# Kernel optimization log

Measured on AMD Instinct MI355X. Metric: run time of the kernel, lower is better.

## Reference

```python
import jax, jax.numpy as jnp
import numpy as np

DIM = 512
NUM_HEADS = 8
HEAD_DIM = DIM // NUM_HEADS
SCALE = HEAD_DIM ** -0.5


def setup_inputs() -> dict:
    key = jax.random.key(0)
    k_x, k_qkv, k_proj, k_pb = jax.random.split(key, 4)
    x = jax.random.normal(k_x, (2, 4096, DIM), dtype=jnp.float32)
    # nn.Linear weights: stored as [out, in]; qkv_bias=False so no qkv bias.
    w_qkv = jax.random.normal(k_qkv, (3 * DIM, DIM), dtype=jnp.float32) * (DIM ** -0.5)
    w_proj = jax.random.normal(k_proj, (DIM, DIM), dtype=jnp.float32) * (DIM ** -0.5)
    b_proj = jax.random.normal(k_pb, (DIM,), dtype=jnp.float32) * 0.01
    return {"x": x, "w_qkv": w_qkv, "w_proj": w_proj, "b_proj": b_proj}


def reference(x, w_qkv, w_proj, b_proj):
    B, N, D = x.shape
    H, Hd = NUM_HEADS, HEAD_DIM
    # qkv: [B, N, 3D] -> [3, B, H, N, Hd]
    qkv = (x @ w_qkv.T).reshape(B, N, 3, H, Hd).transpose(2, 0, 3, 1, 4)
    q, k, v = qkv[0], qkv[1], qkv[2]
    # Naive full attention matrix in fp32 (matches original non-fused path).
    attn = jnp.einsum('bhqd,bhkd->bhqk', q, k) * SCALE
    attn = jax.nn.softmax(attn, axis=-1)
    out = jnp.einsum('bhqk,bhkd->bhqd', attn, v)
    out = out.transpose(0, 2, 1, 3).reshape(B, N, D)
    return out @ w_proj.T + b_proj
```

## Files before the change

### kernel.cpp

```cpp
#include <hip/hip_runtime.h>
#include <stdint.h>

#define SEQ   4096
#define DIMM  512
#define HDIM  64
#define NH    8
#define ROWS  8192
#define QKVN  1536

typedef __attribute__((ext_vector_type(8))) __bf16 bf16x8;
typedef __attribute__((ext_vector_type(4))) float  f32x4;
typedef __attribute__((ext_vector_type(2))) uint32_t u32x2;

__device__ __forceinline__ uint16_t f2bfu(float f) {
  uint32_t u = __builtin_bit_cast(uint32_t, f);
  return (uint16_t)((u + 0x7FFFu + ((u >> 16) & 1u)) >> 16);
}

__device__ __forceinline__ f32x4 mfma16(bf16x8 a, bf16x8 b, f32x4 c) {
  return __builtin_amdgcn_mfma_f32_16x16x32_bf16(a, b, c, 0, 0, 0);
}

#if __has_builtin(__builtin_amdgcn_exp2f)
#define EXP2F(x) __builtin_amdgcn_exp2f(x)
#else
#define EXP2F(x) exp2f(x)
#endif

__device__ __forceinline__ void gld16(const void* g, void* l) {
  __builtin_amdgcn_global_load_lds(
      (const __attribute__((address_space(1))) uint32_t*)g,
      (__attribute__((address_space(3))) uint32_t*)l, 16, 0, 0);
}

#define X4  (ROWS * DIMM / 4)
#define Q4  (QKVN * DIMM / 4)
#define P4  (DIMM * DIMM / 4)

__global__ __launch_bounds__(256) void cvt_kernel(
    const float* __restrict__ x, const float* __restrict__ wq,
    const float* __restrict__ wp, uint16_t* __restrict__ xb,
    uint16_t* __restrict__ wqb, uint16_t* __restrict__ wpb) {
  int idx = blockIdx.x * 256 + threadIdx.x;
  const float* src; uint16_t* dst; int i4;
  if (idx < X4)            { src = x;  dst = xb;  i4 = idx; }
  else if (idx < X4 + Q4)  { src = wq; dst = wqb; i4 = idx - X4; }
  else                     { src = wp; dst = wpb; i4 = idx - X4 - Q4; }
  float4 v = ((const float4*)src)[i4];
  ushort4 o;
  o.x = f2bfu(v.x); o.y = f2bfu(v.y); o.z = f2bfu(v.z); o.w = f2bfu(v.w);
  ((ushort4*)dst)[i4] = o;
}

__device__ __forceinline__ void gemm_core(
    const uint16_t* __restrict__ A, const uint16_t* __restrict__ B,
    uint16_t* As, uint16_t* Bs, f32x4 acc[4][4]) {
  const int tid = threadIdx.x;
  const int lane = tid & 63, wave = tid >> 6;
  const int quad = lane >> 4, l16 = lane & 15;
  const int wr = (wave & 1) * 64, wc = (wave >> 1) * 64;
  const int bm = blockIdx.x, bn = blockIdx.y;
  const int sw = (l16 >> 1) & 3;

  for (int kt = 0; kt < DIMM / 32; ++kt) {
#pragma unroll
    for (int it = 0; it < 2; ++it) {
      int L = it * 256 + tid;
      int r = L >> 2, c = L & 3;
      int gc = c ^ ((r >> 1) & 3);
      int ldsoff = (it * 256 + (tid & ~63)) * 16;
      gld16((const char*)A + ((size_t)(bm * 128 + r) * DIMM + kt * 32) * 2 + gc * 16,
            (char*)As + ldsoff);
      gld16((const char*)B + ((size_t)(bn * 128 + r) * DIMM + kt * 32) * 2 + gc * 16,
            (char*)Bs + ldsoff);
    }
    __syncthreads();
    bf16x8 af[4], bfr[4];
#pragma unroll
    for (int i = 0; i < 4; ++i)
      af[i] = *(const bf16x8*)(As + (wr + i * 16 + l16) * 32 + ((quad ^ sw) * 8));
#pragma unroll
    for (int j = 0; j < 4; ++j)
      bfr[j] = *(const bf16x8*)(Bs + (wc + j * 16 + l16) * 32 + ((quad ^ sw) * 8));
#pragma unroll
    for (int i = 0; i < 4; ++i)
#pragma unroll
      for (int j = 0; j < 4; ++j)
        acc[i][j] = mfma16(af[i], bfr[j], acc[i][j]);
    __syncthreads();
  }
}

__global__ __launch_bounds__(256, 2) void qkv_gemm(
    const uint16_t* __restrict__ xb, const uint16_t* __restrict__ wqb,
    uint16_t* __restrict__ qd, uint16_t* __restrict__ kd,
    uint16_t* __restrict__ vt) {
  __shared__ __align__(16) uint16_t As[128 * 32];
  __shared__ __align__(16) uint16_t Bs[128 * 32];
  f32x4 acc[4][4];
#pragma unroll
  for (int i = 0; i < 4; ++i)
#pragma unroll
    for (int j = 0; j < 4; ++j) acc[i][j] = f32x4{0.f, 0.f, 0.f, 0.f};

  gemm_core(xb, wqb, As, Bs, acc);

  const int lane = threadIdx.x & 63, wave = threadIdx.x >> 6;
  const int quad = lane >> 4, l16 = lane & 15;
  const int wr = (wave & 1) * 64, wc = (wave >> 1) * 64;
  const float qscale = 0.125f * 1.44269504f;
#pragma unroll
  for (int i = 0; i < 4; ++i) {
    int m0 = blockIdx.x * 128 + wr + i * 16 + quad * 4;
    int b = m0 >> 12, n0 = m0 & 4095;
#pragma unroll
    for (int j = 0; j < 4; ++j) {
      int jc = blockIdx.y * 128 + wc + j * 16 + l16;
      int region = jc >> 9;
      int h = (jc >> 6) & 7, hd = jc & 63;
      int bh = (b << 3) | h;
      if (region == 0) {
#pragma unroll
        for (int r = 0; r < 4; ++r)
          qd[((size_t)bh * SEQ + n0 + r) * HDIM + hd] = f2bfu(acc[i][j][r] * qscale);
      } else if (region == 1) {
#pragma unroll
        for (int r = 0; r < 4; ++r)
          kd[((size_t)bh * SEQ + n0 + r) * HDIM + hd] = f2bfu(acc[i][j][r]);
      } else {
        ushort4 pk;
        pk.x = f2bfu(acc[i][j][0]); pk.y = f2bfu(acc[i][j][1]);
        pk.z = f2bfu(acc[i][j][2]); pk.w = f2bfu(acc[i][j][3]);
        *(ushort4*)(vt + ((size_t)bh * HDIM + hd) * SEQ + n0) = pk;
      }
    }
  }
}

__global__ __launch_bounds__(512, 4) void attn_kernel(
    const uint16_t* __restrict__ qd, const uint16_t* __restrict__ kd,
    const uint16_t* __restrict__ vt, uint16_t* __restrict__ ao) {
  __shared__ __align__(16) uint16_t Ks[128 * 64];
  __shared__ __align__(16) uint16_t Vs[64 * 128];
  __shared__ __align__(16) uint16_t Ps[8][32 * 64];

  const int tid = threadIdx.x, lane = tid & 63, wave = tid >> 6;
  const int quad = lane >> 4, l16 = lane & 15;
  const int pair = wave >> 1, khalf = wave & 1;
  const int qt = blockIdx.x, bh = blockIdx.y;
  const size_t base_qk = (size_t)bh * SEQ * HDIM;
  const size_t base_v  = (size_t)bh * HDIM * SEQ;
  const int sw7 = l16 & 7;
  char* Pw = (char*)Ps + wave * 4096;

  bf16x8 qf[2][2];
#pragma unroll
  for (int it2 = 0; it2 < 2; ++it2)
#pragma unroll
    for (int kh = 0; kh < 2; ++kh)
      qf[it2][kh] = *(const bf16x8*)(qd + base_qk +
          (size_t)(qt * 128 + pair * 32 + it2 * 16 + l16) * HDIM + kh * 32 + quad * 8);

  f32x4 O[2][4];
  float lsum[2] = {0.f, 0.f};
#pragma unroll
  for (int a = 0; a < 2; ++a)
#pragma unroll
    for (int d = 0; d < 4; ++d) O[a][d] = f32x4{0.f, 0.f, 0.f, 0.f};

  for (int kt = 0; kt < SEQ / 128; ++kt) {
#pragma unroll
    for (int it = 0; it < 2; ++it) {
      int L = it * 512 + tid;
      int ldsoff = (it * 512 + (tid & ~63)) * 16;
      int rk = L >> 3, ck = L & 7;
      int gck = ck ^ (rk & 7);
      gld16((const char*)kd + (base_qk + (size_t)(kt * 128 + rk) * HDIM) * 2 + gck * 16,
            (char*)Ks + ldsoff);
      int rv = L >> 4, cv = L & 15;
      int gcv = cv ^ (rv & 15);
      gld16((const char*)vt + (base_v + (size_t)rv * SEQ + (size_t)kt * 128) * 2 + gcv * 16,
            (char*)Vs + ldsoff);
    }
    __syncthreads();

    f32x4 P[4][2];
#pragma unroll
    for (int jh = 0; jh < 4; ++jh) {
      int jf = khalf * 4 + jh;
      const uint16_t* krow = Ks + (jf * 16 + l16) * 64;
      bf16x8 kf0 = *(const bf16x8*)(krow + ((quad ^ sw7) * 8));
      bf16x8 kf1 = *(const bf16x8*)(krow + (((4 + quad) ^ sw7) * 8));
#pragma unroll
      for (int it2 = 0; it2 < 2; ++it2) {
        f32x4 s = f32x4{0.f, 0.f, 0.f, 0.f};
        s = mfma16(kf0, qf[it2][0], s);
        s = mfma16(kf1, qf[it2][1], s);
        P[jh][it2] = s;
      }
    }

#pragma unroll
    for (int jh = 0; jh < 4; ++jh)
#pragma unroll
      for (int it2 = 0; it2 < 2; ++it2) {
        float p0 = EXP2F(P[jh][it2][0]);
        float p1 = EXP2F(P[jh][it2][1]);
        float p2 = EXP2F(P[jh][it2][2]);
        float p3 = EXP2F(P[jh][it2][3]);
        lsum[it2] += (p0 + p1) + (p2 + p3);
        uint32_t a0 = __builtin_bit_cast(uint32_t, p0) + 0x8000u;
        uint32_t a1 = __builtin_bit_cast(uint32_t, p1) + 0x8000u;
        uint32_t a2 = __builtin_bit_cast(uint32_t, p2) + 0x8000u;
        uint32_t a3 = __builtin_bit_cast(uint32_t, p3) + 0x8000u;
        u32x2 pk;
        pk.x = (a0 >> 16) | (a1 & 0xFFFF0000u);
        pk.y = (a2 >> 16) | (a3 & 0xFFFF0000u);
        int c16 = (jh * 2 + (quad >> 1)) ^ sw7;
        *(u32x2*)(Pw + (it2 * 16 + l16) * 128 + c16 * 16 + (quad & 1) * 8) = pk;
      }

#pragma unroll
    for (int kp = 0; kp < 2; ++kp) {
      bf16x8 pb[2];
#pragma unroll
      for (int it2 = 0; it2 < 2; ++it2)
        pb[it2] = *(const bf16x8*)(Pw + (it2 * 16 + l16) * 128 +
                                   (((kp * 4 + quad) ^ sw7) * 16));
      bf16x8 va[4];
#pragma unroll
      for (int dl = 0; dl < 4; ++dl)
        va[dl] = *(const bf16x8*)((const char*)Vs + (dl * 16 + l16) * 256 +
                                  (((khalf * 8 + kp * 4 + quad) ^ l16) & 15) * 16);
#pragma unroll
      for (int it2 = 0; it2 < 2; ++it2)
#pragma unroll
        for (int dl = 0; dl < 4; ++dl)
          O[it2][dl] = mfma16(va[dl], pb[it2], O[it2][dl]);
    }
    __syncthreads();
  }

  if (!(wave & 1)) {
    f32x4* ob = (f32x4*)((char*)Ps + wave * 4096);
#pragma unroll
    for (int it2 = 0; it2 < 2; ++it2)
#pragma unroll
      for (int dl = 0; dl < 4; ++dl)
        ob[(it2 * 4 + dl) * 64 + lane] = O[it2][dl];
    float2* lb = (float2*)((char*)Ks + pair * 512);
    lb[lane] = make_float2(lsum[0], lsum[1]);
  }
  __syncthreads();
  if (wave & 1) {
    const f32x4* ob = (const f32x4*)((char*)Ps + (wave - 1) * 4096);
    float2 lp = ((const float2*)((char*)Ks + pair * 512))[lane];
    lsum[0] += lp.x; lsum[1] += lp.y;
#pragma unroll
    for (int it2 = 0; it2 < 2; ++it2)
#pragma unroll
      for (int dl = 0; dl < 4; ++dl)
        O[it2][dl] += ob[(it2 * 4 + dl) * 64 + lane];

    const int b = bh >> 3, h = bh & 7;
#pragma unroll
    for (int it2 = 0; it2 < 2; ++it2) {
      float l = lsum[it2];
      l += __shfl_xor(l, 16);
      l += __shfl_xor(l, 32);
      float inv = 1.0f / l;
      int q = qt * 128 + pair * 32 + it2 * 16 + l16;
      size_t rowbase = ((size_t)(b * SEQ + q)) * DIMM + h * HDIM;
#pragma unroll
      for (int dl = 0; dl < 4; ++dl) {
        ushort4 pk;
        pk.x = f2bfu(O[it2][dl][0] * inv);
        pk.y = f2bfu(O[it2][dl][1] * inv);
        pk.z = f2bfu(O[it2][dl][2] * inv);
        pk.w = f2bfu(O[it2][dl][3] * inv);
        *(ushort4*)(ao + rowbase + dl * 16 + quad * 4) = pk;
      }
    }
  }
}

__global__ __launch_bounds__(256, 2) void proj_gemm(
    const uint16_t* __restrict__ ao, const uint16_t* __restrict__ wpb,
    const float* __restrict__ bprj, float* __restrict__ out) {
  __shared__ __align__(16) uint16_t As[128 * 32];
  __shared__ __align__(16) uint16_t Bs[128 * 32];
  f32x4 acc[4][4];
#pragma unroll
  for (int i = 0; i < 4; ++i)
#pragma unroll
    for (int j = 0; j < 4; ++j) acc[i][j] = f32x4{0.f, 0.f, 0.f, 0.f};

  gemm_core(ao, wpb, As, Bs, acc);

  const int lane = threadIdx.x & 63, wave = threadIdx.x >> 6;
  const int quad = lane >> 4, l16 = lane & 15;
  const int wr = (wave & 1) * 64, wc = (wave >> 1) * 64;
#pragma unroll
  for (int i = 0; i < 4; ++i) {
    int m0 = blockIdx.x * 128 + wr + i * 16 + quad * 4;
#pragma unroll
    for (int j = 0; j < 4; ++j) {
      int jc = blockIdx.y * 128 + wc + j * 16 + l16;
      float bias = bprj[jc];
#pragma unroll
      for (int r = 0; r < 4; ++r)
        out[(size_t)(m0 + r) * DIMM + jc] = acc[i][j][r] + bias;
    }
  }
}

extern "C" void kernel_launch(void* const* d_in, const int* in_sizes, int n_in,
                              void* d_out, int out_size, void* d_ws, size_t ws_size,
                              hipStream_t stream) {
  const float* x     = (const float*)d_in[0];
  const float* wqkv  = (const float*)d_in[1];
  const float* wproj = (const float*)d_in[2];
  const float* bproj = (const float*)d_in[3];

  char* ws = (char*)d_ws;
  uint16_t* xb  = (uint16_t*)(ws + 0);
  uint16_t* wqb = (uint16_t*)(ws + 8388608);
  uint16_t* wpb = (uint16_t*)(ws + 9961472);
  uint16_t* qd  = (uint16_t*)(ws + 10485760);
  uint16_t* kd  = (uint16_t*)(ws + 18874368);
  uint16_t* vt  = (uint16_t*)(ws + 27262976);
  uint16_t* ao  = (uint16_t*)(ws + 35651584);

  cvt_kernel<<<(X4 + Q4 + P4) / 256, 256, 0, stream>>>(x, wqkv, wproj, xb, wqb, wpb);
  qkv_gemm<<<dim3(64, 12), 256, 0, stream>>>(xb, wqb, qd, kd, vt);
  attn_kernel<<<dim3(32, 16), 512, 0, stream>>>(qd, kd, vt, ao);
  proj_gemm<<<dim3(64, 4), 256, 0, stream>>>(ao, wpb, bproj, (float*)d_out);
}
```

Measured before the change: 195.1 us.

## Split QKV GEMM, transpose operands for vector stores, read K directly from global

The QKV projection is split into a Q/K GEMM with swapped operands and a separate V GEMM, so Q/K outputs are written as packed 4-element stores instead of scalar strided stores. The projection GEMM likewise swaps operands to emit float4 output stores with vectorized bias loads. The attention kernel drops the LDS staging of K tiles and loads K fragments straight from global memory, and reorders the grid so heads are the fastest-varying index. Direct global K loads lose the async LDS prefetch and may raise load latency in the attention inner loop.

New measurement: 247.4 us. 1.27x slower.

```diff
diff --git a/kernel.cpp b/kernel.cpp
--- a/kernel.cpp
+++ b/kernel.cpp
@@ -91,9 +91,45 @@
   }
 }
 
-__global__ __launch_bounds__(256, 2) void qkv_gemm(
+__global__ __launch_bounds__(256, 2) void qk_gemm(
     const uint16_t* __restrict__ xb, const uint16_t* __restrict__ wqb,
-    uint16_t* __restrict__ qd, uint16_t* __restrict__ kd,
+    uint16_t* __restrict__ qd, uint16_t* __restrict__ kd) {
+  __shared__ __align__(16) uint16_t As[128 * 32];
+  __shared__ __align__(16) uint16_t Bs[128 * 32];
+  f32x4 acc[4][4];
+#pragma unroll
+  for (int i = 0; i < 4; ++i)
+#pragma unroll
+    for (int j = 0; j < 4; ++j) acc[i][j] = f32x4{0.f, 0.f, 0.f, 0.f};
+
+  gemm_core(wqb, xb, As, Bs, acc);
+
+  const int lane = threadIdx.x & 63, wave = threadIdx.x >> 6;
+  const int quad = lane >> 4, l16 = lane & 15;
+  const int wr = (wave & 1) * 64, wc = (wave >> 1) * 64;
+  const float qscale = 0.125f * 1.44269504f;
+  const bool isq = (blockIdx.x < 4);
+  uint16_t* dst = isq ? qd : kd;
+  const float s = isq ? qscale : 1.0f;
+#pragma unroll
+  for (int i = 0; i < 4; ++i) {
+    int jc0 = blockIdx.x * 128 + wr + i * 16 + quad * 4;
+    int h = (jc0 >> 6) & 7, hd = jc0 & 63;
+#pragma unroll
+    for (int j = 0; j < 4; ++j) {
+      int m = blockIdx.y * 128 + wc + j * 16 + l16;
+      int b = m >> 12, n = m & 4095;
+      int bh = (b << 3) | h;
+      ushort4 pk;
+      pk.x = f2bfu(acc[i][j][0] * s); pk.y = f2bfu(acc[i][j][1] * s);
+      pk.z = f2bfu(acc[i][j][2] * s); pk.w = f2bfu(acc[i][j][3] * s);
+      *(ushort4*)(dst + ((size_t)bh * SEQ + n) * HDIM + hd) = pk;
+    }
+  }
+}
+
+__global__ __launch_bounds__(256, 2) void v_gemm(
+    const uint16_t* __restrict__ xb, const uint16_t* __restrict__ wvb,
     uint16_t* __restrict__ vt) {
   __shared__ __align__(16) uint16_t As[128 * 32];
   __shared__ __align__(16) uint16_t Bs[128 * 32];
@@ -103,36 +139,24 @@
 #pragma unroll
     for (int j = 0; j < 4; ++j) acc[i][j] = f32x4{0.f, 0.f, 0.f, 0.f};
 
-  gemm_core(xb, wqb, As, Bs, acc);
+  gemm_core(xb, wvb, As, Bs, acc);
 
   const int lane = threadIdx.x & 63, wave = threadIdx.x >> 6;
   const int quad = lane >> 4, l16 = lane & 15;
   const int wr = (wave & 1) * 64, wc = (wave >> 1) * 64;
-  const float qscale = 0.125f * 1.44269504f;
 #pragma unroll
   for (int i = 0; i < 4; ++i) {
     int m0 = blockIdx.x * 128 + wr + i * 16 + quad * 4;
     int b = m0 >> 12, n0 = m0 & 4095;
 #pragma unroll
     for (int j = 0; j < 4; ++j) {
-      int jc = blockIdx.y * 128 + wc + j * 16 + l16;
-      int region = jc >> 9;
-      int h = (jc >> 6) & 7, hd = jc & 63;
+      int jcl = blockIdx.y * 128 + wc + j * 16 + l16;
+      int h = (jcl >> 6) & 7, hd = jcl & 63;
       int bh = (b << 3) | h;
-      if (region == 0) {
-#pragma unroll
-        for (int r = 0; r < 4; ++r)
-          qd[((size_t)bh * SEQ + n0 + r) * HDIM + hd] = f2bfu(acc[i][j][r] * qscale);
-      } else if (region == 1) {
-#pragma unroll
-        for (int r = 0; r < 4; ++r)
-          kd[((size_t)bh * SEQ + n0 + r) * HDIM + hd] = f2bfu(acc[i][j][r]);
-      } else {
-        ushort4 pk;
-        pk.x = f2bfu(acc[i][j][0]); pk.y = f2bfu(acc[i][j][1]);
-        pk.z = f2bfu(acc[i][j][2]); pk.w = f2bfu(acc[i][j][3]);
-        *(ushort4*)(vt + ((size_t)bh * HDIM + hd) * SEQ + n0) = pk;
-      }
+      ushort4 pk;
+      pk.x = f2bfu(acc[i][j][0]); pk.y = f2bfu(acc[i][j][1]);
+      pk.z = f2bfu(acc[i][j][2]); pk.w = f2bfu(acc[i][j][3]);
+      *(ushort4*)(vt + ((size_t)bh * HDIM + hd) * SEQ + n0) = pk;
     }
   }
 }
@@ -140,14 +164,14 @@
 __global__ __launch_bounds__(512, 4) void attn_kernel(
     const uint16_t* __restrict__ qd, const uint16_t* __restrict__ kd,
     const uint16_t* __restrict__ vt, uint16_t* __restrict__ ao) {
-  __shared__ __align__(16) uint16_t Ks[128 * 64];
   __shared__ __align__(16) uint16_t Vs[64 * 128];
   __shared__ __align__(16) uint16_t Ps[8][32 * 64];
+  __shared__ __align__(16) float2 Lb[4 * 64];
 
   const int tid = threadIdx.x, lane = tid & 63, wave = tid >> 6;
   const int quad = lane >> 4, l16 = lane & 15;
   const int pair = wave >> 1, khalf = wave & 1;
-  const int qt = blockIdx.x, bh = blockIdx.y;
+  const int qt = blockIdx.x >> 4, bh = blockIdx.x & 15;
   const size_t base_qk = (size_t)bh * SEQ * HDIM;
   const size_t base_v  = (size_t)bh * HDIM * SEQ;
   const int sw7 = l16 & 7;
@@ -173,10 +197,6 @@
     for (int it = 0; it < 2; ++it) {
       int L = it * 512 + tid;
       int ldsoff = (it * 512 + (tid & ~63)) * 16;
-      int rk = L >> 3, ck = L & 7;
-      int gck = ck ^ (rk & 7);
-      gld16((const char*)kd + (base_qk + (size_t)(kt * 128 + rk) * HDIM) * 2 + gck * 16,
-            (char*)Ks + ldsoff);
       int rv = L >> 4, cv = L & 15;
       int gcv = cv ^ (rv & 15);
       gld16((const char*)vt + (base_v + (size_t)rv * SEQ + (size_t)kt * 128) * 2 + gcv * 16,
@@ -188,9 +208,10 @@
 #pragma unroll
     for (int jh = 0; jh < 4; ++jh) {
       int jf = khalf * 4 + jh;
-      const uint16_t* krow = Ks + (jf * 16 + l16) * 64;
-      bf16x8 kf0 = *(const bf16x8*)(krow + ((quad ^ sw7) * 8));
-      bf16x8 kf1 = *(const bf16x8*)(krow + (((4 + quad) ^ sw7) * 8));
+      const uint16_t* krow = kd + base_qk +
+          (size_t)(kt * 128 + jf * 16 + l16) * HDIM;
+      bf16x8 kf0 = *(const bf16x8*)(krow + quad * 8);
+      bf16x8 kf1 = *(const bf16x8*)(krow + 32 + quad * 8);
 #pragma unroll
       for (int it2 = 0; it2 < 2; ++it2) {
         f32x4 s = f32x4{0.f, 0.f, 0.f, 0.f};
@@ -248,13 +269,12 @@
 #pragma unroll
       for (int dl = 0; dl < 4; ++dl)
         ob[(it2 * 4 + dl) * 64 + lane] = O[it2][dl];
-    float2* lb = (float2*)((char*)Ks + pair * 512);
-    lb[lane] = make_float2(lsum[0], lsum[1]);
+    Lb[pair * 64 + lane] = make_float2(lsum[0], lsum[1]);
   }
   __syncthreads();
   if (wave & 1) {
     const f32x4* ob = (const f32x4*)((char*)Ps + (wave - 1) * 4096);
-    float2 lp = ((const float2*)((char*)Ks + pair * 512))[lane];
+    float2 lp = Lb[pair * 64 + lane];
     lsum[0] += lp.x; lsum[1] += lp.y;
 #pragma unroll
     for (int it2 = 0; it2 < 2; ++it2)
@@ -295,21 +315,22 @@
 #pragma unroll
     for (int j = 0; j < 4; ++j) acc[i][j] = f32x4{0.f, 0.f, 0.f, 0.f};
 
-  gemm_core(ao, wpb, As, Bs, acc);
+  gemm_core(wpb, ao, As, Bs, acc);
 
   const int lane = threadIdx.x & 63, wave = threadIdx.x >> 6;
   const int quad = lane >> 4, l16 = lane & 15;
   const int wr = (wave & 1) * 64, wc = (wave >> 1) * 64;
 #pragma unroll
   for (int i = 0; i < 4; ++i) {
-    int m0 = blockIdx.x * 128 + wr + i * 16 + quad * 4;
+    int jc0 = blockIdx.x * 128 + wr + i * 16 + quad * 4;
+    float4 b4 = *(const float4*)(bprj + jc0);
 #pragma unroll
     for (int j = 0; j < 4; ++j) {
-      int jc = blockIdx.y * 128 + wc + j * 16 + l16;
-      float bias = bprj[jc];
-#pragma unroll
-      for (int r = 0; r < 4; ++r)
-        out[(size_t)(m0 + r) * DIMM + jc] = acc[i][j][r] + bias;
+      int m = blockIdx.y * 128 + wc + j * 16 + l16;
+      float4 o;
+      o.x = acc[i][j][0] + b4.x; o.y = acc[i][j][1] + b4.y;
+      o.z = acc[i][j][2] + b4.z; o.w = acc[i][j][3] + b4.w;
+      *(float4*)(out + (size_t)m * DIMM + jc0) = o;
     }
   }
 }
@@ -332,7 +353,8 @@
   uint16_t* ao  = (uint16_t*)(ws + 35651584);
 
   cvt_kernel<<<(X4 + Q4 + P4) / 256, 256, 0, stream>>>(x, wqkv, wproj, xb, wqb, wpb);
-  qkv_gemm<<<dim3(64, 12), 256, 0, stream>>>(xb, wqb, qd, kd, vt);
-  attn_kernel<<<dim3(32, 16), 512, 0, stream>>>(qd, kd, vt, ao);
-  proj_gemm<<<dim3(64, 4), 256, 0, stream>>>(ao, wpb, bproj, (float*)d_out);
-}
+  qk_gemm<<<dim3(8, 64), 256, 0, stream>>>(xb, wqb, qd, kd);
+  v_gemm<<<dim3(64, 4), 256, 0, stream>>>(xb, wqb + 1024 * DIMM, vt);
+  attn_kernel<<<512, 512, 0, stream>>>(qd, kd, vt, ao);
+  proj_gemm<<<dim3(4, 64), 256, 0, stream>>>(ao, wpb, bproj, (float*)d_out);
+}
```
